# Optimization experiments

Measured on AMD Instinct MI355X. Metric: run time of the kernel, lower is better.

The kernel has to match this reference:

```python
import jax, jax.numpy as jnp
from jax import lax
import numpy as np

B, T, IN_DIM = 32, 2048, 36
HIDDEN, CODE_DIM, N_CODES, STRIDE, N_RES = 256, 128, 1024, 4, 4
BETA = 0.25
GN_GROUPS = 8


def conv1d(x, w, b, stride=1, padding=0):
    # x: (B,C,T), w: (O,I,k) torch layout
    y = lax.conv_general_dilated(x, w, (stride,), [(padding, padding)],
                                 dimension_numbers=('NCH', 'OIH', 'NCH'))
    return y + b[None, :, None]


def conv_transpose1d(x, w, b, stride, padding):
    # torch ConvTranspose1d weight layout (in, out, k); output_padding=0 (stride even)
    k = w.shape[-1]
    w_t = jnp.transpose(jnp.flip(w, -1), (1, 0, 2))  # (out, in, k)
    y = lax.conv_general_dilated(x, w_t, (1,), [(k - 1 - padding, k - 1 - padding)],
                                 lhs_dilation=(stride,), dimension_numbers=('NCH', 'OIH', 'NCH'))
    return y + b[None, :, None]


def group_norm(x, gamma, beta, eps=1e-5):
    Bx, C, Tx = x.shape
    xg = x.reshape(Bx, GN_GROUPS, C // GN_GROUPS, Tx)
    mu = xg.mean(axis=(2, 3), keepdims=True)
    var = xg.var(axis=(2, 3), keepdims=True)
    xn = ((xg - mu) * lax.rsqrt(var + eps)).reshape(Bx, C, Tx)
    return xn * gamma[None, :, None] + beta[None, :, None]


def res_block(x, g1, be1, w1, b1, g2, be2, w2, b2):
    h = conv1d(jax.nn.silu(group_norm(x, g1, be1)), w1, b1, padding=1)
    h = conv1d(jax.nn.silu(group_norm(h, g2, be2)), w2, b2, padding=1)
    return x + h


def vq(z_e, codebook):
    # z_e: (B, C, K); nearest-neighbor + straight-through estimator
    Bx, C, K = z_e.shape
    z = z_e.transpose(0, 2, 1).reshape(-1, C)  # (B*K, C)
    dist = (z * z).sum(1, keepdims=True) + (codebook * codebook).sum(1)[None, :] - 2.0 * (z @ codebook.T)
    codes = jnp.argmin(dist, axis=1)  # (B*K,)
    z_q = codebook[codes].reshape(Bx, K, C).transpose(0, 2, 1)  # (B, C, K)
    z_q_st = z_e + lax.stop_gradient(z_q - z_e)
    loss_vq = jnp.mean((z_q - lax.stop_gradient(z_e)) ** 2) + BETA * jnp.mean((lax.stop_gradient(z_q) - z_e) ** 2)
    counts = jnp.zeros((N_CODES,), z_e.dtype).at[codes].add(1.0)
    avg = counts / z.shape[0]
    perplexity = jnp.exp(-jnp.sum(avg * jnp.log(avg + 1e-10)))
    return z_q_st, codes.reshape(Bx, K), loss_vq, perplexity


def _gather_pos(a):  # slices (0:18),(18:21),(27:30) -> 24 dims
    return jnp.concatenate([a[..., 0:18], a[..., 18:21], a[..., 27:30]], axis=-1)


def _gather_dir(a):  # slices (21:27),(30:36) -> 12 dims
    return jnp.concatenate([a[..., 21:27], a[..., 30:36]], axis=-1)


def setup_inputs() -> dict:
    ks = iter(jax.random.split(jax.random.key(0), 64))

    def nrm(shape, scale=1.0):
        return scale * jax.random.normal(next(ks), shape, jnp.float32)

    def cw(o, i, k):
        return nrm((o, i, k), 1.0 / np.sqrt(i * k))

    def rcw(n, o, i, k):
        return nrm((n, o, i, k), 1.0 / np.sqrt(i * k))

    inp = {
        'x': nrm((B, T, IN_DIM)),
        'hand_valid_mask': jax.random.uniform(next(ks), (B, T, 2), jnp.float32),
        'enc_in_w': cw(HIDDEN, IN_DIM, 3), 'enc_in_b': nrm((HIDDEN,), 0.01),
        'enc_gn1_g': 1.0 + nrm((N_RES, HIDDEN), 0.01), 'enc_gn1_b': nrm((N_RES, HIDDEN), 0.01),
        'enc_c1_w': rcw(N_RES, HIDDEN, HIDDEN, 3), 'enc_c1_b': nrm((N_RES, HIDDEN), 0.01),
        'enc_gn2_g': 1.0 + nrm((N_RES, HIDDEN), 0.01), 'enc_gn2_b': nrm((N_RES, HIDDEN), 0.01),
        'enc_c2_w': rcw(N_RES, HIDDEN, HIDDEN, 3), 'enc_c2_b': nrm((N_RES, HIDDEN), 0.01),
        'down_w': cw(HIDDEN, HIDDEN, 2 * STRIDE), 'down_b': nrm((HIDDEN,), 0.01),
        'enc_out_w': cw(CODE_DIM, HIDDEN, 1), 'enc_out_b': nrm((CODE_DIM,), 0.01),
        'codebook': jax.random.uniform(next(ks), (N_CODES, CODE_DIM), jnp.float32, -1.0 / N_CODES, 1.0 / N_CODES),
        'dec_in_w': cw(HIDDEN, CODE_DIM, 1), 'dec_in_b': nrm((HIDDEN,), 0.01),
        'up_w': nrm((HIDDEN, HIDDEN, 2 * STRIDE), 1.0 / np.sqrt(HIDDEN * 2 * STRIDE)), 'up_b': nrm((HIDDEN,), 0.01),
        'dec_gn1_g': 1.0 + nrm((N_RES, HIDDEN), 0.01), 'dec_gn1_b': nrm((N_RES, HIDDEN), 0.01),
        'dec_c1_w': rcw(N_RES, HIDDEN, HIDDEN, 3), 'dec_c1_b': nrm((N_RES, HIDDEN), 0.01),
        'dec_gn2_g': 1.0 + nrm((N_RES, HIDDEN), 0.01), 'dec_gn2_b': nrm((N_RES, HIDDEN), 0.01),
        'dec_c2_w': rcw(N_RES, HIDDEN, HIDDEN, 3), 'dec_c2_b': nrm((N_RES, HIDDEN), 0.01),
        'dec_out_w': cw(IN_DIM, HIDDEN, 3), 'dec_out_b': nrm((IN_DIM,), 0.01),
    }
    return inp


def reference(x, hand_valid_mask, enc_in_w, enc_in_b, enc_gn1_g, enc_gn1_b, enc_c1_w, enc_c1_b,
              enc_gn2_g, enc_gn2_b, enc_c2_w, enc_c2_b, down_w, down_b, enc_out_w, enc_out_b,
              codebook, dec_in_w, dec_in_b, up_w, up_b, dec_gn1_g, dec_gn1_b, dec_c1_w, dec_c1_b,
              dec_gn2_g, dec_gn2_b, dec_c2_w, dec_c2_b, dec_out_w, dec_out_b):
    Bx, Tx, _ = x.shape
    # ---- encode ----
    h = conv1d(x.transpose(0, 2, 1), enc_in_w, enc_in_b, padding=1)
    for i in range(N_RES):
        h = res_block(h, enc_gn1_g[i], enc_gn1_b[i], enc_c1_w[i], enc_c1_b[i],
                      enc_gn2_g[i], enc_gn2_b[i], enc_c2_w[i], enc_c2_b[i])
    h = conv1d(h, down_w, down_b, stride=STRIDE, padding=STRIDE // 2)
    z_e = conv1d(h, enc_out_w, enc_out_b)  # (B, CODE_DIM, K); latent mask is all-ones (no input_length)
    # ---- quantize ----
    z_q, codes, loss_vq, perplexity = vq(z_e, codebook)
    # ---- decode ----
    h = conv1d(z_q, dec_in_w, dec_in_b)
    h = conv_transpose1d(h, up_w, up_b, STRIDE, STRIDE // 2)
    for i in range(N_RES):
        h = res_block(h, dec_gn1_g[i], dec_gn1_b[i], dec_c1_w[i], dec_c1_b[i],
                      dec_gn2_g[i], dec_gn2_b[i], dec_c2_w[i], dec_c2_b[i])
    x_hat = conv1d(h, dec_out_w, dec_out_b, padding=1)[..., :Tx].transpose(0, 2, 1)  # (B,T,36)
    # ---- smooth-L1 position loss (mask of ones (B,T,1): denom = B*T) ----
    d = _gather_pos(x_hat) - _gather_pos(x)
    ad = jnp.abs(d)
    l1 = jnp.where(ad < 1.0, 0.5 * d * d, ad - 0.5)
    loss_recon_pos = l1.sum() / (Bx * Tx)
    # ---- cosine direction loss with hand validity mask ----
    x_vec = _gather_dir(x).reshape(Bx, Tx, 4, 3)
    h_vec = _gather_dir(x_hat).reshape(Bx, Tx, 4, 3)
    mL = hand_valid_mask[..., 0]
    mR = hand_valid_mask[..., 1]
    m_vec = jnp.stack([mL, mL, mR, mR], axis=-1)  # (B,T,4)
    eps = 1e-8
    xn = x_vec / (jnp.linalg.norm(x_vec, axis=-1, keepdims=True) + eps)
    hn = h_vec / (jnp.linalg.norm(h_vec, axis=-1, keepdims=True) + eps)
    cos = (xn * hn).sum(-1)
    loss_recon_dir = ((1.0 - cos) * m_vec).sum() / jnp.maximum(m_vec.sum(), 1.0)
    return x_hat, codes, loss_vq, perplexity, loss_recon_pos, loss_recon_dir
```

## Files before the change

### kernel.cpp

```cpp
#include <hip/hip_runtime.h>
#include <cstddef>
#include <cstdint>


#define TID ((int)threadIdx.x)
#define NB 32

__device__ __forceinline__ float silu_f(float y) { return y / (1.f + expf(-y)); }

__global__ void perm_oik_iko(const float* __restrict__ src, float* __restrict__ dst,
                             int R, int O, int I, int K) {
  int n = R * O * I * K;
  for (int idx = blockIdx.x * blockDim.x + TID; idx < n; idx += gridDim.x * blockDim.x) {
    int o = idx % O;
    int k = (idx / O) % K;
    int i = (idx / (O * K)) % I;
    int r = idx / (O * K * I);
    dst[idx] = src[((r * O + o) * I + i) * K + k];
  }
}

__global__ void perm_decout(const float* __restrict__ src, float* __restrict__ dst) {
  int n = 256 * 36 * 4;
  for (int idx = blockIdx.x * blockDim.x + TID; idx < n; idx += gridDim.x * blockDim.x) {
    int k = idx & 3;
    int o = (idx >> 2) % 36;
    int i = idx / 144;
    dst[idx] = (k < 3) ? src[(o * 256 + i) * 3 + k] : 0.f;
  }
}

__global__ void zero_k(float* p, int n) {
  int i = blockIdx.x * blockDim.x + TID;
  if (i < n) p[i] = 0.f;
}

__global__ void csq_f32(const float* __restrict__ cb, float* __restrict__ csq) {
  int j = blockIdx.x * blockDim.x + TID;
  if (j < 1024) {
    float s = 0.f;
    for (int c = 0; c < 128; c++) { float v = cb[j * 128 + c]; s += v * v; }
    csq[j] = s;
  }
}

__global__ __launch_bounds__(256) void conv_in_k(const float* __restrict__ x, const float* __restrict__ wT,
                                                 const float* __restrict__ bias, float* __restrict__ out,
                                                 float* __restrict__ partOut) {
  int b = blockIdx.x >> 5;
  int t0 = (blockIdx.x & 31) << 6;
  int o0 = blockIdx.y << 6;
  int tx = TID & 15, oy = TID >> 4;
  __shared__ float ins[36][68];
  __shared__ float wsl[36 * 192];
  for (int idx = TID; idx < 36 * 66; idx += 256) {
    int i = idx % 36, c = idx / 36;
    int t = t0 - 1 + c;
    float v = 0.f;
    if (t >= 0 && t < 2048) v = x[((size_t)(b * 2048 + t)) * 36 + i];
    ins[i][c] = v;
  }
  for (int idx = TID; idx < 36 * 192; idx += 256) {
    int o = idx & 63;
    int kk = (idx >> 6) % 3;
    int i = idx / 192;
    wsl[idx] = wT[(i * 3 + kk) * 256 + o0 + o];
  }
  __syncthreads();
  float acc[4][4];
#pragma unroll
  for (int m = 0; m < 4; m++)
#pragma unroll
    for (int n = 0; n < 4; n++) acc[m][n] = 0.f;
  for (int i = 0; i < 36; i++) {
    float xv[6];
    float4 x4 = *(const float4*)&ins[i][tx << 2];
    xv[0] = x4.x; xv[1] = x4.y; xv[2] = x4.z; xv[3] = x4.w;
    xv[4] = ins[i][(tx << 2) + 4];
    xv[5] = ins[i][(tx << 2) + 5];
    const float* wrow = &wsl[i * 192];
    float wv[3][4];
    *(float4*)wv[0] = *(const float4*)&wrow[oy << 2];
    *(float4*)wv[1] = *(const float4*)&wrow[64 + (oy << 2)];
    *(float4*)wv[2] = *(const float4*)&wrow[128 + (oy << 2)];
#pragma unroll
    for (int m = 0; m < 4; m++)
#pragma unroll
      for (int n = 0; n < 4; n++)
        acc[m][n] += wv[0][m] * xv[n] + wv[1][m] * xv[n + 1] + wv[2][m] * xv[n + 2];
  }
  int obase = o0 + (oy << 2);
  float s1 = 0.f, s2 = 0.f;
#pragma unroll
  for (int m = 0; m < 4; m++) {
    int o = obase + m;
    float bv = bias[o];
    size_t rowo = (((size_t)((b << 8) + o)) << 11) + t0 + (tx << 2);
#pragma unroll
    for (int n = 0; n < 4; n++) {
      float v = acc[m][n] + bv;
      out[rowo + n] = v;
      s1 += v; s2 += v * v;
    }
  }
  __syncthreads();
  float* red = (float*)ins;
  red[TID] = s1; red[256 + TID] = s2;
  __syncthreads();
  for (int st = 64; st > 0; st >>= 1) {
    if ((TID & 127) < st) { red[TID] += red[TID + st]; red[256 + TID] += red[256 + TID + st]; }
    __syncthreads();
  }
  if ((TID & 127) == 0) {
    int g = (blockIdx.y << 1) + (TID >> 7);
    atomicAdd(&partOut[(((b << 3) + g) << 1)], red[TID]);
    atomicAdd(&partOut[(((b << 3) + g) << 1) + 1], red[256 + TID]);
  }
}

__global__ __launch_bounds__(256, 2) void conv3_gn_k(const float* __restrict__ in, const float* __restrict__ partIn,
                                                     const float* __restrict__ gamma, const float* __restrict__ beta,
                                                     const float* __restrict__ wT, const float* __restrict__ bias,
                                                     const float* __restrict__ src, float* __restrict__ out,
                                                     float* __restrict__ partOut) {
  int b = blockIdx.x >> 3;
  int t0 = (blockIdx.x & 7) << 8;
  int o0 = blockIdx.y << 7;
  int tx = TID & 15, oy = TID >> 4;
  __shared__ float ins[16][264];
  __shared__ float wsl[3 * 16 * 128];
  float acc[2][4][16];
#pragma unroll
  for (int h = 0; h < 2; h++)
#pragma unroll
    for (int m = 0; m < 4; m++)
#pragma unroll
      for (int n = 0; n < 16; n++) acc[h][m][n] = 0.f;

  float xpre[17];
  float4 wpre[6];
  {
    const float* grow = in + (((size_t)((b << 8) + oy)) << 11);
#pragma unroll
    for (int q = 0; q < 17; q++) {
      int c = tx + (q << 4);
      float v = 0.f;
      if (c < 260) {
        int t = t0 - 1 + c;
        if (t >= 0 && t < 2048) v = grow[t];
      }
      xpre[q] = v;
    }
#pragma unroll
    for (int j = 0; j < 6; j++) {
      int idx4 = TID + (j << 8);
      int o4 = (idx4 & 31) << 2;
      int i = (idx4 >> 5) & 15;
      int kk = idx4 >> 9;
      wpre[j] = *(const float4*)&wT[(i * 3 + kk) * 256 + o0 + o4];
    }
  }

  for (int ic0 = 0; ic0 < 256; ic0 += 16) {
    int g = ic0 >> 5;
    const float* pp = partIn + (((size_t)((b << 3) + g)) << 1);
    float s1 = pp[0], s2 = pp[1];
    float mu = s1 * (1.f / 65536.f);
    float var = s2 * (1.f / 65536.f) - mu * mu;
    float rs = rsqrtf(var + 1e-5f);
    int ch = ic0 + oy;
    float a = rs * gamma[ch];
    float bb = beta[ch] - mu * a;
    __syncthreads();
#pragma unroll
    for (int q = 0; q < 17; q++) {
      int c = tx + (q << 4);
      if (c < 260) {
        int t = t0 - 1 + c;
        float v = 0.f;
        if (t >= 0 && t < 2048) {
          float y = xpre[q] * a + bb;
          v = y / (1.f + expf(-y));
        }
        ins[oy][c] = v;
      }
    }
#pragma unroll
    for (int j = 0; j < 6; j++) {
      int idx4 = TID + (j << 8);
      int o4 = (idx4 & 31) << 2;
      int i = (idx4 >> 5) & 15;
      int kk = idx4 >> 9;
      *(float4*)&wsl[(((kk << 4) + i) << 7) + o4] = wpre[j];
    }
    __syncthreads();
    if (ic0 < 240) {
      int icn = ic0 + 16;
      const float* grow = in + (((size_t)((b << 8) + icn + oy)) << 11);
#pragma unroll
      for (int q = 0; q < 17; q++) {
        int c = tx + (q << 4);
        float v = 0.f;
        if (c < 260) {
          int t = t0 - 1 + c;
          if (t >= 0 && t < 2048) v = grow[t];
        }
        xpre[q] = v;
      }
#pragma unroll
      for (int j = 0; j < 6; j++) {
        int idx4 = TID + (j << 8);
        int o4 = (idx4 & 31) << 2;
        int i = (idx4 >> 5) & 15;
        int kk = idx4 >> 9;
        wpre[j] = *(const float4*)&wT[((icn + i) * 3 + kk) * 256 + o0 + o4];
      }
    }
    for (int i = 0; i < 16; i++) {
      float xq[4][6];
#pragma unroll
      for (int q = 0; q < 4; q++) {
        *(float4*)&xq[q][0] = *(const float4*)&ins[i][(q << 6) + (tx << 2)];
        *(float2*)&xq[q][4] = *(const float2*)&ins[i][(q << 6) + (tx << 2) + 4];
      }
      float wv[3][4], wb[3][4];
#pragma unroll
      for (int kk = 0; kk < 3; kk++) {
        const float* wrow = &wsl[((kk << 4) + i) << 7];
        *(float4*)wv[kk] = *(const float4*)&wrow[oy << 2];
        *(float4*)wb[kk] = *(const float4*)&wrow[64 + (oy << 2)];
      }
#pragma unroll
      for (int m = 0; m < 4; m++)
#pragma unroll
        for (int q = 0; q < 4; q++)
#pragma unroll
          for (int n = 0; n < 4; n++) {
            acc[0][m][(q << 2) + n] += wv[0][m] * xq[q][n] + wv[1][m] * xq[q][n + 1] + wv[2][m] * xq[q][n + 2];
            acc[1][m][(q << 2) + n] += wb[0][m] * xq[q][n] + wb[1][m] * xq[q][n + 1] + wb[2][m] * xq[q][n + 2];
          }
    }
  }
  float sh1[2] = {0.f, 0.f}, sh2[2] = {0.f, 0.f};
#pragma unroll
  for (int h = 0; h < 2; h++)
#pragma unroll
    for (int m = 0; m < 4; m++) {
      int o = o0 + (h << 6) + (oy << 2) + m;
      float bv = bias[o];
      size_t rowbase = (((size_t)((b << 8) + o)) << 11) + t0 + (tx << 2);
#pragma unroll
      for (int q = 0; q < 4; q++) {
        size_t row = rowbase + (q << 6);
#pragma unroll
        for (int n = 0; n < 4; n++) {
          float v = acc[h][m][(q << 2) + n] + bv;
          if (src) v += src[row + n];
          out[row + n] = v;
          sh1[h] += v; sh2[h] += v * v;
        }
      }
    }
  __syncthreads();
  float* red = (float*)ins;
#pragma unroll
  for (int h = 0; h < 2; h++) {
    red[TID] = sh1[h]; red[256 + TID] = sh2[h];
    __syncthreads();
    for (int st = 64; st > 0; st >>= 1) {
      if ((TID & 127) < st) { red[TID] += red[TID + st]; red[256 + TID] += red[256 + TID + st]; }
      __syncthreads();
    }
    if ((TID & 127) == 0) {
      int g = (blockIdx.y << 2) + (h << 1) + (TID >> 7);
      atomicAdd(&partOut[(((b << 3) + g) << 1)], red[TID]);
      atomicAdd(&partOut[(((b << 3) + g) << 1) + 1], red[256 + TID]);
    }
    __syncthreads();
  }
}

__global__ __launch_bounds__(256) void conv_down_k(const float* __restrict__ in, const float* __restrict__ wT,
                                                   const float* __restrict__ bias, float* __restrict__ out) {
  int b = blockIdx.x >> 3;
  int to0 = (blockIdx.x & 7) << 6;
  int o0 = blockIdx.y << 6;
  int tx = TID & 15, oy = TID >> 4;
  __shared__ float ins[16][264];
  __shared__ float wsl[16 * 512];
  float acc[4][4];
#pragma unroll
  for (int m = 0; m < 4; m++)
#pragma unroll
    for (int n = 0; n < 4; n++) acc[m][n] = 0.f;
  for (int ic0 = 0; ic0 < 256; ic0 += 16) {
    __syncthreads();
    for (int idx = TID; idx < 16 * 260; idx += 256) {
      int r = idx / 260, c = idx % 260;
      int s = (to0 << 2) - 2 + c;
      float v = 0.f;
      if (s >= 0 && s < 2048) v = in[(((size_t)((b << 8) + ic0 + r)) << 11) + s];
      ins[r][c] = v;
    }
    for (int idx = TID; idx < 16 * 512; idx += 256) {
      int o = idx & 63;
      int kk = (idx >> 6) & 7;
      int i = idx >> 9;
      wsl[idx] = wT[((ic0 + i) * 8 + kk) * 256 + o0 + o];
    }
    __syncthreads();
#pragma unroll 2
    for (int i = 0; i < 16; i++) {
      float xv[20];
#pragma unroll
      for (int q = 0; q < 5; q++) *(float4*)&xv[q * 4] = *(const float4*)&ins[i][(tx << 4) + (q << 2)];
      float wv[8][4];
#pragma unroll
      for (int kk = 0; kk < 8; kk++) *(float4*)wv[kk] = *(const float4*)&wsl[(i << 9) + (kk << 6) + (oy << 2)];
#pragma unroll
      for (int n = 0; n < 4; n++)
#pragma unroll
        for (int kk = 0; kk < 8; kk++) {
          float xval = xv[(n << 2) + kk];
#pragma unroll
          for (int m = 0; m < 4; m++) acc[m][n] += wv[kk][m] * xval;
        }
    }
  }
  int obase = o0 + (oy << 2);
#pragma unroll
  for (int m = 0; m < 4; m++) {
    int o = obase + m;
    float bv = bias[o];
    size_t rowo = (((size_t)((b << 8) + o)) << 9) + to0 + (tx << 2);
#pragma unroll
    for (int n = 0; n < 4; n++) out[rowo + n] = acc[m][n] + bv;
  }
}

__global__ __launch_bounds__(256) void conv1x1_k(const float* __restrict__ in, const float* __restrict__ wIO,
                                                 const float* __restrict__ bias, float* __restrict__ out,
                                                 int Kc, int O) {
  int b = blockIdx.x >> 3;
  int t0 = (blockIdx.x & 7) << 6;
  int o0 = blockIdx.y << 6;
  int tx = TID & 15, oy = TID >> 4;
  __shared__ float xs[32][64];
  __shared__ float wsd[32][64];
  float acc[4][4];
#pragma unroll
  for (int m = 0; m < 4; m++)
#pragma unroll
    for (int n = 0; n < 4; n++) acc[m][n] = 0.f;
  for (int ic0 = 0; ic0 < Kc; ic0 += 32) {
    __syncthreads();
    for (int idx = TID; idx < 2048; idx += 256) {
      int r = idx >> 6, c = idx & 63;
      xs[r][c] = in[((size_t)(b * Kc + ic0 + r) << 9) + t0 + c];
      wsd[r][c] = wIO[(ic0 + r) * O + o0 + c];
    }
    __syncthreads();
#pragma unroll 8
    for (int i = 0; i < 32; i++) {
      float4 xvv = *(const float4*)&xs[i][tx << 2];
      float4 wvv = *(const float4*)&wsd[i][oy << 2];
      float xv[4] = {xvv.x, xvv.y, xvv.z, xvv.w};
      float wv[4] = {wvv.x, wvv.y, wvv.z, wvv.w};
#pragma unroll
      for (int m = 0; m < 4; m++)
#pragma unroll
        for (int n = 0; n < 4; n++) acc[m][n] += wv[m] * xv[n];
    }
  }
#pragma unroll
  for (int m = 0; m < 4; m++) {
    int o = o0 + (oy << 2) + m;
    float bv = bias[o];
    size_t rowo = ((size_t)(b * O + o) << 9) + t0 + (tx << 2);
#pragma unroll
    for (int n = 0; n < 4; n++) out[rowo + n] = acc[m][n] + bv;
  }
}

__global__ __launch_bounds__(256) void vq_tiled(const float* __restrict__ zE,
                                                const float* __restrict__ cb,
                                                const float* __restrict__ csq,
                                                int* __restrict__ codes) {
  int b = blockIdx.x >> 3;
  int t0 = (blockIdx.x & 7) << 6;
  int cq = TID & 15, pq = TID >> 4;
  __shared__ float Zs[128][66];
  __shared__ float Cs[64][129];
  __shared__ float zsqs[64];
  __shared__ float bd[64][17];
  __shared__ int bix[64][17];
  for (int idx = TID; idx < 128 * 64; idx += 256) {
    int c = idx >> 6, p = idx & 63;
    Zs[c][p] = zE[((size_t)(b * 128 + c) << 9) + t0 + p];
  }
  __syncthreads();
  if (TID < 64) {
    float s = 0.f;
    for (int c = 0; c < 128; c++) { float v = Zs[c][TID]; s += v * v; }
    zsqs[TID] = s;
  }
  float best[4];
  int bidx[4];
#pragma unroll
  for (int n = 0; n < 4; n++) { best[n] = 3.4e38f; bidx[n] = 0; }
  const int j0 = cq << 2;
  for (int cg = 0; cg < 16; cg++) {
    __syncthreads();
    for (int idx = TID; idx < 64 * 128; idx += 256) {
      int j = idx >> 7, c = idx & 127;
      Cs[j][c] = cb[((cg << 6) + j) * 128 + c];
    }
    __syncthreads();
    float acc[4][4];
#pragma unroll
    for (int u = 0; u < 4; u++)
#pragma unroll
      for (int n = 0; n < 4; n++) acc[u][n] = 0.f;
    for (int c = 0; c < 128; c++) {
      float4 zv4 = *(const float4*)&Zs[c][pq << 2];
      float zv[4] = {zv4.x, zv4.y, zv4.z, zv4.w};
      float cv[4];
#pragma unroll
      for (int u = 0; u < 4; u++) cv[u] = Cs[j0 + u][c];
#pragma unroll
      for (int u = 0; u < 4; u++)
#pragma unroll
        for (int n = 0; n < 4; n++) acc[u][n] += zv[n] * cv[u];
    }
#pragma unroll
    for (int u = 0; u < 4; u++) {
      int code = (cg << 6) + j0 + u;
      float cs_ = csq[code];
#pragma unroll
      for (int n = 0; n < 4; n++) {
        float A = zsqs[(pq << 2) + n] + cs_;
        float B = 2.0f * acc[u][n];
        float d = A - B;
        if (d < best[n]) { best[n] = d; bidx[n] = code; }
      }
    }
  }
  __syncthreads();
#pragma unroll
  for (int n = 0; n < 4; n++) { bd[(pq << 2) + n][cq] = best[n]; bix[(pq << 2) + n][cq] = bidx[n]; }
  __syncthreads();
  if (TID < 64) {
    float bb = bd[TID][0];
    int bj = bix[TID][0];
    for (int q = 1; q < 16; q++) {
      float d = bd[TID][q];
      int j = bix[TID][q];
      if (d < bb || (d == bb && j < bj)) { bb = d; bj = j; }
    }
    codes[(b << 9) + t0 + TID] = bj;
  }
}

__global__ void count_k(const int* __restrict__ codes, float* __restrict__ counts) {
  int n = blockIdx.x * blockDim.x + TID;
  if (n < 16384) atomicAdd(&counts[codes[n]], 1.f);
}

__global__ __launch_bounds__(256) void gather_k(const float* __restrict__ cb, const int* __restrict__ codes,
                                                const float* __restrict__ zE, float* __restrict__ zQ,
                                                float* __restrict__ vqsum) {
  double part = 0.;
  const int total = 32 * 128 * 512;
  for (int idx = blockIdx.x * blockDim.x + TID; idx < total; idx += gridDim.x * blockDim.x) {
    int t = idx & 511;
    int c = (idx >> 9) & 127;
    int b = idx >> 16;
    int code = codes[(b << 9) + t];
    float q = cb[code * 128 + c];
    double d = (double)q - (double)zE[idx];
    zQ[idx] = q;
    part += d * d;
  }
  __shared__ double red[256];
  red[TID] = part;
  __syncthreads();
  for (int st = 128; st > 0; st >>= 1) {
    if (TID < st) red[TID] += red[TID + st];
    __syncthreads();
  }
  if (TID == 0) atomicAdd(vqsum, (float)red[0]);
}

__global__ __launch_bounds__(256) void conv_up_k(const float* __restrict__ in, const float* __restrict__ w,
                                                 const float* __restrict__ bias, float* __restrict__ out,
                                                 float* __restrict__ partOut) {
  int b = blockIdx.x / 17;
  int s0 = (blockIdx.x % 17) << 5;
  int o0 = blockIdx.y << 6;
  int tx = TID & 15, oy = TID >> 4;
  __shared__ float ins[16][36];
  __shared__ float wsl[16 * 512];
  float acc[2][4][4];
#pragma unroll
  for (int j = 0; j < 2; j++)
#pragma unroll
    for (int m = 0; m < 4; m++)
#pragma unroll
      for (int r = 0; r < 4; r++) acc[j][m][r] = 0.f;
  for (int ic0 = 0; ic0 < 256; ic0 += 16) {
    __syncthreads();
    for (int idx = TID; idx < 16 * 34; idx += 256) {
      int r = idx / 34, c = idx % 34;
      int s = s0 - 1 + c;
      float v = 0.f;
      if (s >= 0 && s < 512) v = in[(((size_t)((b << 8) + ic0 + r)) << 9) + s];
      ins[r][c] = v;
    }
    for (int idx = TID; idx < 8192; idx += 256) {
      int rr = idx & 3;
      int o = (idx >> 2) & 63;
      int h = (idx >> 8) & 1;
      int i = idx >> 9;
      wsl[idx] = w[(((size_t)(ic0 + i)) << 11) + ((size_t)(o0 + o) << 3) + (h << 2) + rr];
    }
    __syncthreads();
#pragma unroll 2
    for (int i = 0; i < 16; i++) {
      float x0 = ins[i][2 * tx], x1 = ins[i][2 * tx + 1], x2 = ins[i][2 * tx + 2];
#pragma unroll
      for (int m = 0; m < 4; m++) {
        int om = (oy << 2) + m;
        float4 wa4 = *(const float4*)&wsl[(i << 9) + (om << 2)];
        float4 wb4 = *(const float4*)&wsl[(i << 9) + 256 + (om << 2)];
        float wa[4] = {wa4.x, wa4.y, wa4.z, wa4.w};
        float wb[4] = {wb4.x, wb4.y, wb4.z, wb4.w};
#pragma unroll
        for (int r = 0; r < 4; r++) {
          acc[0][m][r] += x1 * wa[r] + x0 * wb[r];
          acc[1][m][r] += x2 * wa[r] + x1 * wb[r];
        }
      }
    }
  }
  float s1 = 0.f, s2 = 0.f;
#pragma unroll
  for (int j = 0; j < 2; j++) {
    int sS = s0 + (tx << 1) + j;
#pragma unroll
    for (int m = 0; m < 4; m++) {
      int o = o0 + (oy << 2) + m;
      float bv = bias[o];
#pragma unroll
      for (int r = 0; r < 4; r++) {
        int t = (sS << 2) + r - 2;
        if (t >= 0 && t < 2048) {
          float v = acc[j][m][r] + bv;
          out[(((size_t)((b << 8) + o)) << 11) + t] = v;
          s1 += v; s2 += v * v;
        }
      }
    }
  }
  __syncthreads();
  float* red = (float*)ins;
  red[TID] = s1; red[256 + TID] = s2;
  __syncthreads();
  for (int st = 64; st > 0; st >>= 1) {
    if ((TID & 127) < st) { red[TID] += red[TID + st]; red[256 + TID] += red[256 + TID + st]; }
    __syncthreads();
  }
  if ((TID & 127) == 0) {
    int g = (blockIdx.y << 1) + (TID >> 7);
    atomicAdd(&partOut[(((b << 3) + g) << 1)], red[TID]);
    atomicAdd(&partOut[(((b << 3) + g) << 1) + 1], red[256 + TID]);
  }
}

__global__ __launch_bounds__(256) void conv_out_k(const float* __restrict__ in, const float* __restrict__ wP,
                                                  const float* __restrict__ bias, float* __restrict__ xhat) {
  int b = blockIdx.x >> 5;
  int t0 = (blockIdx.x & 31) << 6;
  int tx = TID & 63, oy = TID >> 6;
  __shared__ float ins[32][68];
  __shared__ float wsl[32 * 144];
  float acc[9];
#pragma unroll
  for (int m = 0; m < 9; m++) acc[m] = 0.f;
  for (int ic0 = 0; ic0 < 256; ic0 += 32) {
    __syncthreads();
    for (int idx = TID; idx < 32 * 66; idx += 256) {
      int r = idx / 66, c = idx % 66;
      int t = t0 - 1 + c;
      float v = 0.f;
      if (t >= 0 && t < 2048) v = in[(((size_t)((b << 8) + ic0 + r)) << 11) + t];
      ins[r][c] = v;
    }
    for (int idx = TID; idx < 32 * 144; idx += 256) {
      wsl[idx] = wP[ic0 * 144 + idx];
    }
    __syncthreads();
#pragma unroll 4
    for (int i = 0; i < 32; i++) {
      float x0 = ins[i][tx], x1 = ins[i][tx + 1], x2 = ins[i][tx + 2];
#pragma unroll
      for (int m = 0; m < 9; m++) {
        int o = oy * 9 + m;
        float4 wv = *(const float4*)&wsl[(i * 36 + o) << 2];
        acc[m] += wv.x * x0 + wv.y * x1 + wv.z * x2;
      }
    }
  }
  size_t orow = ((size_t)(b << 11) + t0 + tx) * 36;
#pragma unroll
  for (int m = 0; m < 9; m++) {
    int o = oy * 9 + m;
    xhat[orow + o] = acc[m] + bias[o];
  }
}

__global__ __launch_bounds__(256) void loss_k(const float* __restrict__ x, const float* __restrict__ xh,
                                              const float* __restrict__ mask, float* __restrict__ scal) {
  float pos = 0.f, dir = 0.f, ms = 0.f;
  for (int n = blockIdx.x * blockDim.x + TID; n < 65536; n += gridDim.x * blockDim.x) {
    const float* xp = x + (size_t)n * 36;
    const float* hp = xh + (size_t)n * 36;
    float a[36], h[36];
#pragma unroll
    for (int d4 = 0; d4 < 36; d4 += 4) {
      *(float4*)&a[d4] = *(const float4*)&xp[d4];
      *(float4*)&h[d4] = *(const float4*)&hp[d4];
    }
#pragma unroll
    for (int d = 0; d < 36; d++) {
      if (d < 21 || (d >= 27 && d < 30)) {
        float df = h[d] - a[d];
        float ad = fabsf(df);
        pos += (ad < 1.f) ? 0.5f * df * df : ad - 0.5f;
      }
    }
    float mL = mask[2 * (size_t)n], mR = mask[2 * (size_t)n + 1];
    const int vb[4] = {21, 24, 30, 33};
    float mv[4] = {mL, mL, mR, mR};
#pragma unroll
    for (int v = 0; v < 4; v++) {
      int o = vb[v];
      float ax = a[o], ay = a[o + 1], az = a[o + 2];
      float hx = h[o], hy = h[o + 1], hz = h[o + 2];
      float an = sqrtf(ax * ax + ay * ay + az * az) + 1e-8f;
      float hn = sqrtf(hx * hx + hy * hy + hz * hz) + 1e-8f;
      float cs = (ax * hx + ay * hy + az * hz) / (an * hn);
      dir += (1.f - cs) * mv[v];
    }
    ms += 2.f * (mL + mR);
  }
  __shared__ float rp[256], rd[256], rm[256];
  rp[TID] = pos; rd[TID] = dir; rm[TID] = ms;
  __syncthreads();
  for (int st = 128; st > 0; st >>= 1) {
    if (TID < st) { rp[TID] += rp[TID + st]; rd[TID] += rd[TID + st]; rm[TID] += rm[TID + st]; }
    __syncthreads();
  }
  if (TID == 0) {
    atomicAdd(&scal[1], rp[0]);
    atomicAdd(&scal[2], rd[0]);
    atomicAdd(&scal[3], rm[0]);
  }
}

__global__ __launch_bounds__(256) void finalize_k(const float* __restrict__ counts, const float* __restrict__ scal,
                                                  float* __restrict__ tail) {
  __shared__ float red[256];
  float s = 0.f;
  for (int j = TID; j < 1024; j += 256) {
    float avg = counts[j] * (1.f / 16384.f);
    s += avg * logf(avg + 1e-10f);
  }
  red[TID] = s;
  __syncthreads();
  for (int st = 128; st > 0; st >>= 1) {
    if (TID < st) red[TID] += red[TID + st];
    __syncthreads();
  }
  if (TID == 0) {
    tail[0] = 1.25f * scal[0] * (1.f / 2097152.f);
    tail[1] = expf(-red[0]);
    tail[2] = scal[1] * (1.f / 65536.f);
    tail[3] = scal[2] / fmaxf(scal[3], 1.f);
  }
}

__global__ void codesf_k(const int* __restrict__ codes, float* __restrict__ o) {
  int n = blockIdx.x * blockDim.x + TID;
  if (n < 16384) o[n] = (float)codes[n];
}

extern "C" void kernel_launch(void* const* d_in, const int* in_sizes, int n_in,
                              void* d_out, int out_size, void* d_ws, size_t ws_size,
                              hipStream_t stream) {
  const float* x = (const float*)d_in[0];
  const float* mask = (const float*)d_in[1];
  const float* enc_in_w = (const float*)d_in[2];
  const float* enc_in_b = (const float*)d_in[3];
  const float* enc_gn1_g = (const float*)d_in[4];
  const float* enc_gn1_b = (const float*)d_in[5];
  const float* enc_c1_w = (const float*)d_in[6];
  const float* enc_c1_b = (const float*)d_in[7];
  const float* enc_gn2_g = (const float*)d_in[8];
  const float* enc_gn2_b = (const float*)d_in[9];
  const float* enc_c2_w = (const float*)d_in[10];
  const float* enc_c2_b = (const float*)d_in[11];
  const float* down_w = (const float*)d_in[12];
  const float* down_b = (const float*)d_in[13];
  const float* enc_out_w = (const float*)d_in[14];
  const float* enc_out_b = (const float*)d_in[15];
  const float* codebook = (const float*)d_in[16];
  const float* dec_in_w = (const float*)d_in[17];
  const float* dec_in_b = (const float*)d_in[18];
  const float* up_w = (const float*)d_in[19];
  const float* up_b = (const float*)d_in[20];
  const float* dec_gn1_g = (const float*)d_in[21];
  const float* dec_gn1_b = (const float*)d_in[22];
  const float* dec_c1_w = (const float*)d_in[23];
  const float* dec_c1_b = (const float*)d_in[24];
  const float* dec_gn2_g = (const float*)d_in[25];
  const float* dec_gn2_b = (const float*)d_in[26];
  const float* dec_c2_w = (const float*)d_in[27];
  const float* dec_c2_b = (const float*)d_in[28];
  const float* dec_out_w = (const float*)d_in[29];
  const float* dec_out_b = (const float*)d_in[30];

  char* W = (char*)d_ws;
  float* zE = (float*)(W + 0);
  float* zQ = (float*)(W + 8388608);
  int* codes = (int*)(W + 16777216);
  float* counts = (float*)(W + 16842752);
  float* scal = (float*)(W + 16846848);
  float* stats = (float*)(W + 16846880);
  float* csq = (float*)(W + 16883744);
  float* wf_enc_in = (float*)(W + 16887840);
  float* wf_enc_c1 = (float*)(W + 16998432);
  float* wf_enc_c2 = (float*)(W + 20144160);
  float* wf_down = (float*)(W + 23289888);
  float* wf_enc_out = (float*)(W + 25387040);
  float* wf_dec_in = (float*)(W + 25518112);
  float* wf_dec_c1 = (float*)(W + 25649184);
  float* wf_dec_c2 = (float*)(W + 28794912);
  float* wf_dec_out = (float*)(W + 31940640);
  float* f0 = (float*)(W + 50331648);
  float* f2 = (float*)(W + 50331648 + (size_t)67108864);
  float* dech = (float*)(W + 50331648 + 2 * (size_t)67108864);

  dim3 blk(256);
  zero_k<<<dim3(41), blk, 0, stream>>>(counts, 1024 + 8 + 9216);
  perm_oik_iko<<<dim3(128), blk, 0, stream>>>(enc_in_w, wf_enc_in, 1, 256, 36, 3);
  perm_oik_iko<<<dim3(1024), blk, 0, stream>>>(enc_c1_w, wf_enc_c1, 4, 256, 256, 3);
  perm_oik_iko<<<dim3(1024), blk, 0, stream>>>(enc_c2_w, wf_enc_c2, 4, 256, 256, 3);
  perm_oik_iko<<<dim3(1024), blk, 0, stream>>>(down_w, wf_down, 1, 256, 256, 8);
  perm_oik_iko<<<dim3(128), blk, 0, stream>>>(enc_out_w, wf_enc_out, 1, 128, 256, 1);
  perm_oik_iko<<<dim3(128), blk, 0, stream>>>(dec_in_w, wf_dec_in, 1, 256, 128, 1);
  perm_oik_iko<<<dim3(1024), blk, 0, stream>>>(dec_c1_w, wf_dec_c1, 4, 256, 256, 3);
  perm_oik_iko<<<dim3(1024), blk, 0, stream>>>(dec_c2_w, wf_dec_c2, 4, 256, 256, 3);
  perm_decout<<<dim3(64), blk, 0, stream>>>(dec_out_w, wf_dec_out);
  csq_f32<<<dim3(4), blk, 0, stream>>>(codebook, csq);

  conv_in_k<<<dim3(NB * 32, 4), blk, 0, stream>>>(x, wf_enc_in, enc_in_b, f0, stats + 0 * 512);
  for (int i = 0; i < 4; i++) {
    float* sIn = stats + (2 * i) * 512;
    float* sMid = stats + (2 * i + 1) * 512;
    float* sOut = stats + (2 * i + 2) * 512;
    conv3_gn_k<<<dim3(NB * 8, 2), blk, 0, stream>>>(f0, sIn, enc_gn1_g + i * 256, enc_gn1_b + i * 256,
                                                    wf_enc_c1 + i * 196608, enc_c1_b + i * 256, nullptr, f2, sMid);
    conv3_gn_k<<<dim3(NB * 8, 2), blk, 0, stream>>>(f2, sMid, enc_gn2_g + i * 256, enc_gn2_b + i * 256,
                                                    wf_enc_c2 + i * 196608, enc_c2_b + i * 256, f0, f0, sOut);
  }
  conv_down_k<<<dim3(NB * 8, 4), blk, 0, stream>>>(f0, wf_down, down_b, f2);
  conv1x1_k<<<dim3(NB * 8, 2), blk, 0, stream>>>(f2, wf_enc_out, enc_out_b, zE, 256, 128);

  vq_tiled<<<dim3(256), blk, 0, stream>>>(zE, codebook, csq, codes);
  count_k<<<dim3(64), blk, 0, stream>>>(codes, counts);
  gather_k<<<dim3(512), blk, 0, stream>>>(codebook, codes, zE, zQ, &scal[0]);

  float* xhat = (float*)d_out;
  conv1x1_k<<<dim3(NB * 8, 4), blk, 0, stream>>>(zQ, wf_dec_in, dec_in_b, dech, 128, 256);
  conv_up_k<<<dim3(NB * 17, 4), blk, 0, stream>>>(dech, up_w, up_b, f0, stats + 9 * 512);
  for (int i = 0; i < 4; i++) {
    float* sIn = stats + (9 + 2 * i) * 512;
    float* sMid = stats + (10 + 2 * i) * 512;
    float* sOut = stats + (11 + 2 * i) * 512;
    conv3_gn_k<<<dim3(NB * 8, 2), blk, 0, stream>>>(f0, sIn, dec_gn1_g + i * 256, dec_gn1_b + i * 256,
                                                    wf_dec_c1 + i * 196608, dec_c1_b + i * 256, nullptr, f2, sMid);
    conv3_gn_k<<<dim3(NB * 8, 2), blk, 0, stream>>>(f2, sMid, dec_gn2_g + i * 256, dec_gn2_b + i * 256,
                                                    wf_dec_c2 + i * 196608, dec_c2_b + i * 256, f0, f0, sOut);
  }
  conv_out_k<<<dim3(NB * 32), blk, 0, stream>>>(f0, wf_dec_out, dec_out_b, xhat);

  loss_k<<<dim3(256), blk, 0, stream>>>(x, xhat, mask, scal);
  finalize_k<<<dim3(1), blk, 0, stream>>>(counts, scal, (float*)d_out + 2375680);
  codesf_k<<<dim3(64), blk, 0, stream>>>(codes, (float*)d_out + 2359296);
}
```

Measured before the change: 7.988 ms.

## Drop register prefetch in conv3_gn_k, use explicit fmaf, skip unused final stats

Removes the register-held prefetch of the next input-channel slice and weight tile in the GroupNorm+conv3 kernel, loading them directly inside the loop instead, which cuts register pressure at the cost of losing load/compute overlap. Rewrites accumulation expressions across conv kernels as explicit fmaf chains. Skips the GroupNorm stats reduction and atomics for the final residual block's output, since nothing reads them.

```diff
diff --git a/kernel.cpp b/kernel.cpp
--- a/kernel.cpp
+++ b/kernel.cpp
@@ -87,7 +87,7 @@
     for (int m = 0; m < 4; m++)
 #pragma unroll
       for (int n = 0; n < 4; n++)
-        acc[m][n] += wv[0][m] * xv[n] + wv[1][m] * xv[n + 1] + wv[2][m] * xv[n + 2];
+        acc[m][n] = fmaf(wv[0][m], xv[n], fmaf(wv[1][m], xv[n + 1], fmaf(wv[2][m], xv[n + 2], acc[m][n])));
   }
   int obase = o0 + (oy << 2);
   float s1 = 0.f, s2 = 0.f;
@@ -136,31 +136,6 @@
     for (int m = 0; m < 4; m++)
 #pragma unroll
       for (int n = 0; n < 16; n++) acc[h][m][n] = 0.f;
-
-  float xpre[17];
-  float4 wpre[6];
-  {
-    const float* grow = in + (((size_t)((b << 8) + oy)) << 11);
-#pragma unroll
-    for (int q = 0; q < 17; q++) {
-      int c = tx + (q << 4);
-      float v = 0.f;
-      if (c < 260) {
-        int t = t0 - 1 + c;
-        if (t >= 0 && t < 2048) v = grow[t];
-      }
-      xpre[q] = v;
-    }
-#pragma unroll
-    for (int j = 0; j < 6; j++) {
-      int idx4 = TID + (j << 8);
-      int o4 = (idx4 & 31) << 2;
-      int i = (idx4 >> 5) & 15;
-      int kk = idx4 >> 9;
-      wpre[j] = *(const float4*)&wT[(i * 3 + kk) * 256 + o0 + o4];
-    }
-  }
-
   for (int ic0 = 0; ic0 < 256; ic0 += 16) {
     int g = ic0 >> 5;
     const float* pp = partIn + (((size_t)((b << 3) + g)) << 1);
@@ -168,54 +143,35 @@
     float mu = s1 * (1.f / 65536.f);
     float var = s2 * (1.f / 65536.f) - mu * mu;
     float rs = rsqrtf(var + 1e-5f);
-    int ch = ic0 + oy;
-    float a = rs * gamma[ch];
-    float bb = beta[ch] - mu * a;
-    __syncthreads();
-#pragma unroll
-    for (int q = 0; q < 17; q++) {
-      int c = tx + (q << 4);
-      if (c < 260) {
-        int t = t0 - 1 + c;
-        float v = 0.f;
-        if (t >= 0 && t < 2048) {
-          float y = xpre[q] * a + bb;
-          v = y / (1.f + expf(-y));
+    __syncthreads();
+    {
+      int ch = ic0 + oy;
+      float a = rs * gamma[ch];
+      float bb = beta[ch] - mu * a;
+      const float* grow = in + (((size_t)((b << 8) + ch)) << 11);
+#pragma unroll
+      for (int q = 0; q < 17; q++) {
+        int c = tx + (q << 4);
+        if (c < 260) {
+          int t = t0 - 1 + c;
+          float v = 0.f;
+          if (t >= 0 && t < 2048) {
+            float h = grow[t];
+            float y = h * a + bb;
+            v = y / (1.f + expf(-y));
+          }
+          ins[oy][c] = v;
         }
-        ins[oy][c] = v;
-      }
-    }
-#pragma unroll
-    for (int j = 0; j < 6; j++) {
-      int idx4 = TID + (j << 8);
+      }
+    }
+    for (int idx4 = TID; idx4 < 1536; idx4 += 256) {
       int o4 = (idx4 & 31) << 2;
       int i = (idx4 >> 5) & 15;
       int kk = idx4 >> 9;
-      *(float4*)&wsl[(((kk << 4) + i) << 7) + o4] = wpre[j];
-    }
-    __syncthreads();
-    if (ic0 < 240) {
-      int icn = ic0 + 16;
-      const float* grow = in + (((size_t)((b << 8) + icn + oy)) << 11);
-#pragma unroll
-      for (int q = 0; q < 17; q++) {
-        int c = tx + (q << 4);
-        float v = 0.f;
-        if (c < 260) {
-          int t = t0 - 1 + c;
-          if (t >= 0 && t < 2048) v = grow[t];
-        }
-        xpre[q] = v;
-      }
-#pragma unroll
-      for (int j = 0; j < 6; j++) {
-        int idx4 = TID + (j << 8);
-        int o4 = (idx4 & 31) << 2;
-        int i = (idx4 >> 5) & 15;
-        int kk = idx4 >> 9;
-        wpre[j] = *(const float4*)&wT[((icn + i) * 3 + kk) * 256 + o0 + o4];
-      }
-    }
+      *(float4*)&wsl[(((kk << 4) + i) << 7) + o4] =
+          *(const float4*)&wT[((ic0 + i) * 3 + kk) * 256 + o0 + o4];
+    }
+    __syncthreads();
     for (int i = 0; i < 16; i++) {
       float xq[4][6];
 #pragma unroll
@@ -236,8 +192,10 @@
         for (int q = 0; q < 4; q++)
 #pragma unroll
           for (int n = 0; n < 4; n++) {
-            acc[0][m][(q << 2) + n] += wv[0][m] * xq[q][n] + wv[1][m] * xq[q][n + 1] + wv[2][m] * xq[q][n + 2];
-            acc[1][m][(q << 2) + n] += wb[0][m] * xq[q][n] + wb[1][m] * xq[q][n + 1] + wb[2][m] * xq[q][n + 2];
+            acc[0][m][(q << 2) + n] =
+                fmaf(wv[0][m], xq[q][n], fmaf(wv[1][m], xq[q][n + 1], fmaf(wv[2][m], xq[q][n + 2], acc[0][m][(q << 2) + n])));
+            acc[1][m][(q << 2) + n] =
+                fmaf(wb[0][m], xq[q][n], fmaf(wb[1][m], xq[q][n + 1], fmaf(wb[2][m], xq[q][n + 2], acc[1][m][(q << 2) + n])));
           }
     }
   }
@@ -261,22 +219,24 @@
         }
       }
     }
-  __syncthreads();
-  float* red = (float*)ins;
-#pragma unroll
-  for (int h = 0; h < 2; h++) {
-    red[TID] = sh1[h]; red[256 + TID] = sh2[h];
-    __syncthreads();
-    for (int st = 64; st > 0; st >>= 1) {
-      if ((TID & 127) < st) { red[TID] += red[TID + st]; red[256 + TID] += red[256 + TID + st]; }
+  if (partOut) {
+    __syncthreads();
+    float* red = (float*)ins;
+#pragma unroll
+    for (int h = 0; h < 2; h++) {
+      red[TID] = sh1[h]; red[256 + TID] = sh2[h];
       __syncthreads();
-    }
-    if ((TID & 127) == 0) {
-      int g = (blockIdx.y << 2) + (h << 1) + (TID >> 7);
-      atomicAdd(&partOut[(((b << 3) + g) << 1)], red[TID]);
-      atomicAdd(&partOut[(((b << 3) + g) << 1) + 1], red[256 + TID]);
-    }
-    __syncthreads();
+      for (int st = 64; st > 0; st >>= 1) {
+        if ((TID & 127) < st) { red[TID] += red[TID + st]; red[256 + TID] += red[256 + TID + st]; }
+        __syncthreads();
+      }
+      if ((TID & 127) == 0) {
+        int g = (blockIdx.y << 2) + (h << 1) + (TID >> 7);
+        atomicAdd(&partOut[(((b << 3) + g) << 1)], red[TID]);
+        atomicAdd(&partOut[(((b << 3) + g) << 1) + 1], red[256 + TID]);
+      }
+      __syncthreads();
+    }
   }
 }
 
@@ -323,7 +283,7 @@
         for (int kk = 0; kk < 8; kk++) {
           float xval = xv[(n << 2) + kk];
 #pragma unroll
-          for (int m = 0; m < 4; m++) acc[m][n] += wv[kk][m] * xval;
+          for (int m = 0; m < 4; m++) acc[m][n] = fmaf(wv[kk][m], xval, acc[m][n]);
         }
     }
   }
@@ -369,7 +329,7 @@
 #pragma unroll
       for (int m = 0; m < 4; m++)
 #pragma unroll
-        for (int n = 0; n < 4; n++) acc[m][n] += wv[m] * xv[n];
+        for (int n = 0; n < 4; n++) acc[m][n] = fmaf(wv[m], xv[n], acc[m][n]);
     }
   }
 #pragma unroll
@@ -536,8 +496,8 @@
         float wb[4] = {wb4.x, wb4.y, wb4.z, wb4.w};
 #pragma unroll
         for (int r = 0; r < 4; r++) {
-          acc[0][m][r] += x1 * wa[r] + x0 * wb[r];
-          acc[1][m][r] += x2 * wa[r] + x1 * wb[r];
+          acc[0][m][r] = fmaf(x1, wa[r], fmaf(x0, wb[r], acc[0][m][r]));
+          acc[1][m][r] = fmaf(x2, wa[r], fmaf(x1, wb[r], acc[1][m][r]));
         }
       }
     }
@@ -606,7 +566,7 @@
       for (int m = 0; m < 9; m++) {
         int o = oy * 9 + m;
         float4 wv = *(const float4*)&wsl[(i * 36 + o) << 2];
-        acc[m] += wv.x * x0 + wv.y * x1 + wv.z * x2;
+        acc[m] = fmaf(wv.x, x0, fmaf(wv.y, x1, fmaf(wv.z, x2, acc[m])));
       }
     }
   }
@@ -767,7 +727,7 @@
   for (int i = 0; i < 4; i++) {
     float* sIn = stats + (2 * i) * 512;
     float* sMid = stats + (2 * i + 1) * 512;
-    float* sOut = stats + (2 * i + 2) * 512;
+    float* sOut = (i < 3) ? stats + (2 * i + 2) * 512 : nullptr;
     conv3_gn_k<<<dim3(NB * 8, 2), blk, 0, stream>>>(f0, sIn, enc_gn1_g + i * 256, enc_gn1_b + i * 256,
                                                     wf_enc_c1 + i * 196608, enc_c1_b + i * 256, nullptr, f2, sMid);
     conv3_gn_k<<<dim3(NB * 8, 2), blk, 0, stream>>>(f2, sMid, enc_gn2_g + i * 256, enc_gn2_b + i * 256,
@@ -786,7 +746,7 @@
   for (int i = 0; i < 4; i++) {
     float* sIn = stats + (9 + 2 * i) * 512;
     float* sMid = stats + (10 + 2 * i) * 512;
-    float* sOut = stats + (11 + 2 * i) * 512;
+    float* sOut = (i < 3) ? stats + (11 + 2 * i) * 512 : nullptr;
     conv3_gn_k<<<dim3(NB * 8, 2), blk, 0, stream>>>(f0, sIn, dec_gn1_g + i * 256, dec_gn1_b + i * 256,
                                                     wf_dec_c1 + i * 196608, dec_c1_b + i * 256, nullptr, f2, sMid);
     conv3_gn_k<<<dim3(NB * 8, 2), blk, 0, stream>>>(f2, sMid, dec_gn2_g + i * 256, dec_gn2_b + i * 256,
```

New measurement: 6.664 ms. -16.6%, faster.
